# Kernel optimization log

Hardware: AMD Instinct MI355X
Metric: run time of the kernel (lower is better)

Reference implementation:

```python
import jax, jax.numpy as jnp
import numpy as np

# ---- equation / net constants (mirrors eqn_config / net_config) ----
NT = 256
DT = 0.04
N_HIST = 64
HIDDEN = 512
LAMBD = 1.0
MU1 = 0.08
MU2 = 0.02
R = 0.02
SIGMA = 0.2
BETA = 0.1
ETA = 0.5
LOGEPS = 1e-6
UTIL_PENALTY = 100.0
GEOMETRIC_SUM = (1.0 - np.exp(-LAMBD * DT * (N_HIST - 1))) / LAMBD  # discounted weight on oldest point
FINAL_DISC = float(np.exp(-BETA * NT * DT))


def setup_inputs() -> dict:
    key = jax.random.key(0)
    k = jax.random.split(key, 9)
    B = 16384
    dw_sample = jax.random.normal(k[0], (B, NT), dtype=jnp.float32) * np.sqrt(DT)
    x_init = jax.random.uniform(k[1], (B, N_HIST), dtype=jnp.float32) + 0.5  # positive initial wealth path
    # exponential kernel over the delay window (most recent point has weight ~1)
    exp_array = jnp.exp(-LAMBD * DT * jnp.arange(N_HIST - 1, 0, -1, dtype=jnp.float32))
    s1 = 1.0 / np.sqrt(N_HIST)
    s2 = 1.0 / np.sqrt(HIDDEN)
    W1 = jax.random.normal(k[2], (N_HIST, HIDDEN), dtype=jnp.float32) * s1
    b1 = jnp.zeros((HIDDEN,), dtype=jnp.float32)
    W2 = jax.random.normal(k[3], (HIDDEN, HIDDEN), dtype=jnp.float32) * s2
    b2 = jnp.zeros((HIDDEN,), dtype=jnp.float32)
    W3 = jax.random.normal(k[4], (HIDDEN, 2), dtype=jnp.float32) * s2
    b3 = jnp.zeros((2,), dtype=jnp.float32)
    return {"dw_sample": dw_sample, "x_init": x_init, "exp_array": exp_array,
            "W1": W1, "b1": b1, "W2": W2, "b2": b2, "W3": W3, "b3": b3}


def reference(dw_sample, x_init, exp_array, W1, b1, W2, b2, W3, b3):
    def util(v):  # log-utility with floor (util_tf)
        return jnp.log(jax.nn.relu(v) + LOGEPS)

    def policy(x_hist):  # feedforward policy on the history window; final_pi_tf = 2*sigmoid
        h = jax.nn.relu(x_hist @ W1 + b1)
        h = jax.nn.relu(h @ W2 + b2)
        return 2.0 * jax.nn.sigmoid(h @ W3 + b3)  # [B, 2]

    x = x_init[:, -1]                       # [B]
    x_hist0 = x_init                        # [B, N_HIST]
    y0 = jnp.sum(exp_array * x_init[:, 1:], axis=-1) * DT + GEOMETRIC_SUM * x_init[:, 0]
    reward0 = jnp.zeros_like(x)

    discounts = jnp.exp(-BETA * DT * jnp.arange(NT, dtype=jnp.float32))  # exp(-beta*t*dt)

    def step(carry, inputs):
        x, y, x_hist, reward = carry
        dw_t, disc = inputs                 # dw_t: [B], disc: scalar
        pi = policy(x_hist)                 # [B, 2]
        inst_r = util(pi[:, 0] * x) * disc - jax.nn.relu(-x) * UTIL_PENALTY
        reward = reward + inst_r * DT
        dx = ((MU1 - R) * pi[:, 1] - pi[:, 0] + R) * x + MU2 * y
        x_new = x + dx * DT + SIGMA * x * pi[:, 1] * dw_t
        y_new = y * jnp.exp(-DT * LAMBD) + x_new * DT
        x_hist_new = jnp.concatenate([x_hist[:, 1:], x_new[:, None]], axis=-1)
        return (x_new, y_new, x_hist_new, reward), None

    (x, y, _, reward), _ = jax.lax.scan(
        step, (x, y0, x_hist0, reward0), (dw_sample.T, discounts))

    # terminal step t == nt
    reward = reward + util(x + ETA * y) / BETA * FINAL_DISC
    reward = reward - jax.nn.relu(-x) * UTIL_PENALTY
    return -reward
```

## Files before the change

### kernel.cpp

```cpp
#include <hip/hip_runtime.h>
#include <stdint.h>
#include <stddef.h>

#define NTS 256

typedef short bf16x8 __attribute__((ext_vector_type(8)));
typedef short bf16x4 __attribute__((ext_vector_type(4)));
typedef float f32x4 __attribute__((ext_vector_type(4)));
typedef float f32x2 __attribute__((ext_vector_type(2)));

__device__ __forceinline__ unsigned short f2bf(float f) {
  union { float f; unsigned u; } c; c.f = f;
  unsigned u = c.u;
  u += 0x7fffu + ((u >> 16) & 1u);
  return (unsigned short)(u >> 16);
}

__global__ __launch_bounds__(256) void prep_weights(const float* __restrict__ W1,
                                                    const float* __restrict__ W2,
                                                    unsigned short* __restrict__ wp) {
  int gid = blockIdx.x * 256 + threadIdx.x;
  if (gid >= 294912) return;
  int e = gid & 7, lane = (gid >> 3) & 63, fb = (gid >> 9) & 31, pan = gid >> 14;
  int q = lane >> 4, j = lane & 15, f = fb * 16 + j;
  float v;
  if (pan < 2) v = W1[(pan * 32 + q * 8 + e) * 512 + f];
  else         v = W2[((pan - 2) * 32 + q * 8 + e) * 512 + f];
  wp[gid] = f2bf(v);
}

__device__ __forceinline__ void stage_panel(const unsigned short* __restrict__ wp,
                                            int pan, char* dst_base, int wv, int lane) {
#pragma unroll
  for (int i = 0; i < 4; ++i) {
    const unsigned short* g = wp + (size_t)pan * 16384 + (wv * 4 + i) * 512 + lane * 8;
    char* l = dst_base + wv * 4096 + i * 1024;
    __builtin_amdgcn_global_load_lds((const __attribute__((address_space(1))) void*)g,
                                     (__attribute__((address_space(3))) void*)l,
                                     16, 0, 0);
  }
}

__global__ __launch_bounds__(512, 2) void po_fused(
    const float* __restrict__ dw, const float* __restrict__ x_init,
    const float* __restrict__ exp_arr, const float* __restrict__ b1,
    const float* __restrict__ b2, const float* __restrict__ W3,
    const float* __restrict__ b3, const unsigned short* __restrict__ wp,
    float* __restrict__ out) {
  extern __shared__ char smem[];
  char* const w1L = smem;
  char* const h1C = smem + 65536;
  char* const histC = smem + 131072;
  unsigned int* const h0L = (unsigned int*)(smem + 139264);
  float* const p0L = (float*)(smem + 143360);
  float* const p1L = (float*)(smem + 145408);
  float* const dwL = (float*)(smem + 147456);
  float* const b1L = (float*)(smem + 151552);
  float* const b2L = (float*)(smem + 153600);
  float* const w3L = (float*)(smem + 155648);

  const int tid = threadIdx.x;
  const int lane = tid & 63;
  const int wv = tid >> 6;
  const int q = lane >> 4;
  const int j = lane & 15;
  const int wg = blockIdx.x;

  b1L[tid] = b1[tid];
  b2L[tid] = b2[tid];
  w3L[tid] = W3[tid];
  w3L[tid + 512] = W3[tid + 512];

  const int b_h = (wv & 3) * 16 + j;
  {
    const int k0 = (wv >> 2) * 32 + q * 8;
    const float* src = x_init + ((size_t)wg * 64 + b_h) * 64 + k0;
    bf16x8 v;
#pragma unroll
    for (int e = 0; e < 8; ++e) v[e] = (short)f2bf(src[e]);
    *(bf16x8*)(histC + tid * 16) = v;
    h0L[tid] = (unsigned int)(unsigned short)v[0];
  }

  float xreg, yreg, rreg = 0.f;
  {
    const float* row = x_init + ((size_t)wg * 64 + lane) * 64;
    float y0 = 0.f;
    for (int k = 0; k < 63; ++k) y0 += exp_arr[k] * row[1 + k];
    yreg = y0 * 0.04f + (1.f - __expf(-2.52f)) * row[0];
    xreg = row[63];
  }
  const float b30 = b3[0], b31 = b3[1];

  stage_panel(wp, 0, w1L, wv, lane);
  stage_panel(wp, 1, w1L + 32768, wv, lane);

  const unsigned short* const wpW2 = wp + 32768;
  const int wfo = wv * 2048 + lane * 8;

  bf16x8 wA[4], wB[4];
#pragma unroll
  for (int mt = 0; mt < 4; ++mt)
    wA[mt] = *(const bf16x8*)(wpW2 + wfo + mt * 512);

  __syncthreads();

  f32x4 acc[4][4];

#pragma unroll 1
  for (int t = 0; t < NTS; ++t) {
    if ((t & 15) == 0) {
      int b = tid >> 3, c = tid & 7;
      f32x2 v = *(const f32x2*)(dw + ((size_t)wg * 64 + b) * NTS + t + c * 2);
      dwL[(c * 2) * 64 + b] = v[0];
      dwL[(c * 2 + 1) * 64 + b] = v[1];
    }

#pragma unroll
    for (int mt = 0; mt < 4; ++mt)
#pragma unroll
      for (int nt = 0; nt < 4; ++nt) acc[mt][nt] = (f32x4){0.f, 0.f, 0.f, 0.f};
#pragma unroll
    for (int p = 0; p < 2; ++p) {
      const char* pb = w1L + p * 32768 + wv * 4096;
      bf16x8 bfr[4];
#pragma unroll
      for (int nt = 0; nt < 4; ++nt)
        bfr[nt] = *(const bf16x8*)(histC + ((p * 4 + nt) * 64 + lane) * 16);
#pragma unroll
      for (int mt = 0; mt < 4; ++mt) {
        bf16x8 afr = *(const bf16x8*)(pb + mt * 1024 + lane * 16);
#pragma unroll
        for (int nt = 0; nt < 4; ++nt)
          acc[mt][nt] = __builtin_amdgcn_mfma_f32_16x16x32_bf16(afr, bfr[nt],
                                                                acc[mt][nt], 0, 0, 0);
      }
    }
#pragma unroll
    for (int mt = 0; mt < 4; ++mt) {
      int f0 = wv * 64 + mt * 16 + q * 4;
      f32x4 b1v = *(const f32x4*)(b1L + f0);
      int wb = ((f0 >> 5) * 256 + ((f0 >> 3) & 3) * 16 + j) * 16 + (f0 & 7) * 2;
#pragma unroll
      for (int nt = 0; nt < 4; ++nt) {
        bf16x4 pk;
#pragma unroll
        for (int r = 0; r < 4; ++r)
          pk[r] = (short)f2bf(fmaxf(acc[mt][nt][r] + b1v[r], 0.f));
        *(bf16x4*)(h1C + wb + nt * 1024) = pk;
      }
    }
    __syncthreads();

#pragma unroll
    for (int mt = 0; mt < 4; ++mt)
#pragma unroll
      for (int nt = 0; nt < 4; ++nt) acc[mt][nt] = (f32x4){0.f, 0.f, 0.f, 0.f};
    {
      const unsigned short* pb = wpW2;
      const char* h1p = h1C;
#pragma unroll 1
      for (int kk = 0; kk < 8; ++kk) {
#pragma unroll
        for (int mt = 0; mt < 4; ++mt)
          wB[mt] = *(const bf16x8*)(pb + 16384 + wfo + mt * 512);
        __builtin_amdgcn_s_setprio(1);
#pragma unroll
        for (int nt = 0; nt < 4; ++nt) {
          bf16x8 bfr = *(const bf16x8*)(h1p + nt * 1024 + lane * 16);
#pragma unroll
          for (int mt = 0; mt < 4; ++mt)
            acc[mt][nt] = __builtin_amdgcn_mfma_f32_16x16x32_bf16(wA[mt], bfr,
                                                                  acc[mt][nt], 0, 0, 0);
        }
        __builtin_amdgcn_s_setprio(0);
        {
          const unsigned short* pn = (kk == 7) ? wpW2 : (pb + 32768);
#pragma unroll
          for (int mt = 0; mt < 4; ++mt)
            wA[mt] = *(const bf16x8*)(pn + wfo + mt * 512);
        }
        __builtin_amdgcn_s_setprio(1);
#pragma unroll
        for (int nt = 0; nt < 4; ++nt) {
          bf16x8 bfr = *(const bf16x8*)(h1p + 4096 + nt * 1024 + lane * 16);
#pragma unroll
          for (int mt = 0; mt < 4; ++mt)
            acc[mt][nt] = __builtin_amdgcn_mfma_f32_16x16x32_bf16(wB[mt], bfr,
                                                                  acc[mt][nt], 0, 0, 0);
        }
        __builtin_amdgcn_s_setprio(0);
        pb += 32768;
        h1p += 8192;
      }
    }

    {
      float p0a[4] = {0.f, 0.f, 0.f, 0.f};
      float p1a[4] = {0.f, 0.f, 0.f, 0.f};
#pragma unroll
      for (int mt = 0; mt < 4; ++mt) {
        int f0 = wv * 64 + mt * 16 + q * 4;
        f32x4 b2v = *(const f32x4*)(b2L + f0);
        f32x4 w3a = *(const f32x4*)(w3L + f0 * 2);
        f32x4 w3b = *(const f32x4*)(w3L + f0 * 2 + 4);
#pragma unroll
        for (int nt = 0; nt < 4; ++nt) {
          float v0 = fmaxf(acc[mt][nt][0] + b2v[0], 0.f);
          float v1 = fmaxf(acc[mt][nt][1] + b2v[1], 0.f);
          float v2 = fmaxf(acc[mt][nt][2] + b2v[2], 0.f);
          float v3 = fmaxf(acc[mt][nt][3] + b2v[3], 0.f);
          p0a[nt] += v0 * w3a[0] + v1 * w3a[2] + v2 * w3b[0] + v3 * w3b[2];
          p1a[nt] += v0 * w3a[1] + v1 * w3a[3] + v2 * w3b[1] + v3 * w3b[3];
        }
      }
#pragma unroll
      for (int nt = 0; nt < 4; ++nt) {
        p0a[nt] += __shfl_xor(p0a[nt], 16);
        p0a[nt] += __shfl_xor(p0a[nt], 32);
        p1a[nt] += __shfl_xor(p1a[nt], 16);
        p1a[nt] += __shfl_xor(p1a[nt], 32);
        if (q == 0) {
          int b = nt * 16 + j;
          p0L[wv * 64 + b] = p0a[nt];
          p1L[wv * 64 + b] = p1a[nt];
        }
      }
    }
    __syncthreads();

    float xn;
    {
      float z0 = b30, z1 = b31;
#pragma unroll
      for (int w = 0; w < 8; ++w) {
        z0 += p0L[w * 64 + lane];
        z1 += p1L[w * 64 + lane];
      }
      float pi0 = 2.f / (1.f + __expf(-z0));
      float pi1 = 2.f / (1.f + __expf(-z1));
      float x = xreg, y = yreg;
      float disc = __expf(-0.004f * (float)t);
      float rv = fmaxf(pi0 * x, 0.f) + 1e-6f;
      rreg += (__logf(rv) * disc - fmaxf(-x, 0.f) * 100.f) * 0.04f;
      float dwv = dwL[(t & 15) * 64 + lane];
      float dxv = (0.06f * pi1 - pi0 + 0.02f) * x + 0.02f * y;
      xn = x + dxv * 0.04f + 0.2f * x * pi1 * dwv;
      yreg = y * 0.960789439152323f + xn * 0.04f;
      xreg = xn;
    }

    {
      bf16x8 own = *(const bf16x8*)(histC + tid * 16);
      int e0 = (int)(unsigned short)own[0];
      int nbr = __shfl_down(e0, 16);
      float xb = __shfl(xn, b_h);
      unsigned short xbf = f2bf(xb);
      unsigned short last;
      if (q == 3) {
        last = (wv >= 4) ? xbf
                         : (unsigned short)h0L[(t & 1) * 512 + tid + 208];
      } else {
        last = (unsigned short)nbr;
      }
      bf16x8 nw;
#pragma unroll
      for (int e = 0; e < 7; ++e) nw[e] = own[e + 1];
      nw[7] = (short)last;
      *(bf16x8*)(histC + tid * 16) = nw;
      h0L[((t + 1) & 1) * 512 + tid] = (unsigned int)(unsigned short)nw[0];
    }
    __syncthreads();
  }

  if (tid < 64) {
    float rw = rreg + __logf(fmaxf(xreg + 0.5f * yreg, 0.f) + 1e-6f) * 10.f * __expf(-1.024f);
    rw -= fmaxf(-xreg, 0.f) * 100.f;
    out[(size_t)wg * 64 + tid] = -rw;
  }
}

extern "C" void kernel_launch(void* const* d_in, const int* in_sizes, int n_in,
                              void* d_out, int out_size, void* d_ws, size_t ws_size,
                              hipStream_t stream) {
  const float* dw      = (const float*)d_in[0];
  const float* x_init  = (const float*)d_in[1];
  const float* exp_arr = (const float*)d_in[2];
  const float* W1      = (const float*)d_in[3];
  const float* b1      = (const float*)d_in[4];
  const float* W2      = (const float*)d_in[5];
  const float* b2      = (const float*)d_in[6];
  const float* W3      = (const float*)d_in[7];
  const float* b3      = (const float*)d_in[8];
  unsigned short* wp = (unsigned short*)d_ws;
  float* out = (float*)d_out;

  (void)hipFuncSetAttribute((const void*)po_fused,
                            hipFuncAttributeMaxDynamicSharedMemorySize, 160 * 1024);

  prep_weights<<<1152, 256, 0, stream>>>(W1, W2, wp);
  po_fused<<<256, 512, 159744, stream>>>(dw, x_init, exp_arr, b1, b2, W3, b3, wp, out);
}
```

Before: 2.271 ms.

## Split W2 GEMM into two half-M passes with 4-deep weight register ring

Layer 1 is reorganized per m-tile so each tile's bias/ReLU/bf16 pack runs right after its MFMAs, and the pack uses the hardware v_cvt_pk_bf16_f32 instruction instead of software rounding. The layer-2 GEMM is split into two passes over K, each covering two of the four m-tiles, with a 4-deep ring of W2 fragments loaded from global/L2 in flight. This hides weight-load latency better. During the second pass the W3 output fold of the first half's finished accumulators is interleaved between MFMA groups, overlapping VALU work with matrix work. The cost is reading the h1 activations from LDS twice and using more registers for the deeper weight ring, which could reduce occupancy.

```diff
diff --git a/kernel.cpp b/kernel.cpp
--- a/kernel.cpp
+++ b/kernel.cpp
@@ -8,12 +8,19 @@
 typedef short bf16x4 __attribute__((ext_vector_type(4)));
 typedef float f32x4 __attribute__((ext_vector_type(4)));
 typedef float f32x2 __attribute__((ext_vector_type(2)));
+typedef unsigned int u32x2 __attribute__((ext_vector_type(2)));
 
 __device__ __forceinline__ unsigned short f2bf(float f) {
   union { float f; unsigned u; } c; c.f = f;
   unsigned u = c.u;
   u += 0x7fffu + ((u >> 16) & 1u);
   return (unsigned short)(u >> 16);
+}
+
+__device__ __forceinline__ unsigned cvt_pk_bf16(float lo, float hi) {
+  unsigned r;
+  asm("v_cvt_pk_bf16_f32 %0, %1, %2" : "=v"(r) : "v"(lo), "v"(hi));
+  return r;
 }
 
 __global__ __launch_bounds__(256) void prep_weights(const float* __restrict__ W1,
@@ -40,6 +47,19 @@
                                      16, 0, 0);
   }
 }
+
+#define FOLD_CHUNK(MT, NT) do {                                              \
+  int f0c = wv * 64 + (MT) * 16 + q * 4;                                     \
+  f32x4 b2v = *(const f32x4*)(b2L + f0c);                                    \
+  f32x4 w3a = *(const f32x4*)(w3L + f0c * 2);                                \
+  f32x4 w3b = *(const f32x4*)(w3L + f0c * 2 + 4);                            \
+  float v0 = fmaxf(acc[MT][NT][0] + b2v[0], 0.f);                            \
+  float v1 = fmaxf(acc[MT][NT][1] + b2v[1], 0.f);                            \
+  float v2 = fmaxf(acc[MT][NT][2] + b2v[2], 0.f);                            \
+  float v3 = fmaxf(acc[MT][NT][3] + b2v[3], 0.f);                            \
+  p0a[NT] += v0 * w3a[0] + v1 * w3a[2] + v2 * w3b[0] + v3 * w3b[2];          \
+  p1a[NT] += v0 * w3a[1] + v1 * w3a[3] + v2 * w3b[1] + v3 * w3b[3];          \
+} while (0)
 
 __global__ __launch_bounds__(512, 2) void po_fused(
     const float* __restrict__ dw, const float* __restrict__ x_init,
@@ -98,10 +118,12 @@
   const unsigned short* const wpW2 = wp + 32768;
   const int wfo = wv * 2048 + lane * 8;
 
-  bf16x8 wA[4], wB[4];
-#pragma unroll
-  for (int mt = 0; mt < 4; ++mt)
-    wA[mt] = *(const bf16x8*)(wpW2 + wfo + mt * 512);
+  bf16x8 wq[4][2];
+#pragma unroll
+  for (int b = 0; b < 4; ++b) {
+    wq[b][0] = *(const bf16x8*)(wpW2 + b * 16384 + wfo);
+    wq[b][1] = *(const bf16x8*)(wpW2 + b * 16384 + wfo + 512);
+  }
 
   __syncthreads();
 
@@ -116,115 +138,101 @@
       dwL[(c * 2 + 1) * 64 + b] = v[1];
     }
 
+    {
+      bf16x8 bh[8];
+#pragma unroll
+      for (int k8 = 0; k8 < 8; ++k8)
+        bh[k8] = *(const bf16x8*)(histC + (k8 * 64 + lane) * 16);
+      const char* pb0 = w1L + wv * 4096;
+#pragma unroll
+      for (int mt = 0; mt < 4; ++mt) {
+        bf16x8 af0 = *(const bf16x8*)(pb0 + mt * 1024 + lane * 16);
+        bf16x8 af1 = *(const bf16x8*)(pb0 + 32768 + mt * 1024 + lane * 16);
+        f32x4 a4[4];
+#pragma unroll
+        for (int nt = 0; nt < 4; ++nt) {
+          a4[nt] = (f32x4){0.f, 0.f, 0.f, 0.f};
+          a4[nt] = __builtin_amdgcn_mfma_f32_16x16x32_bf16(af0, bh[nt], a4[nt], 0, 0, 0);
+          a4[nt] = __builtin_amdgcn_mfma_f32_16x16x32_bf16(af1, bh[4 + nt], a4[nt], 0, 0, 0);
+        }
+        int f0 = wv * 64 + mt * 16 + q * 4;
+        f32x4 b1v = *(const f32x4*)(b1L + f0);
+        int wb = ((f0 >> 5) * 256 + ((f0 >> 3) & 3) * 16 + j) * 16 + (f0 & 7) * 2;
+#pragma unroll
+        for (int nt = 0; nt < 4; ++nt) {
+          f32x4 vv = a4[nt] + b1v;
+          u32x2 pk;
+          pk[0] = cvt_pk_bf16(fmaxf(vv[0], 0.f), fmaxf(vv[1], 0.f));
+          pk[1] = cvt_pk_bf16(fmaxf(vv[2], 0.f), fmaxf(vv[3], 0.f));
+          *(u32x2*)(h1C + wb + nt * 1024) = pk;
+        }
+      }
+    }
+    __syncthreads();
+
 #pragma unroll
     for (int mt = 0; mt < 4; ++mt)
 #pragma unroll
       for (int nt = 0; nt < 4; ++nt) acc[mt][nt] = (f32x4){0.f, 0.f, 0.f, 0.f};
-#pragma unroll
-    for (int p = 0; p < 2; ++p) {
-      const char* pb = w1L + p * 32768 + wv * 4096;
-      bf16x8 bfr[4];
-#pragma unroll
-      for (int nt = 0; nt < 4; ++nt)
-        bfr[nt] = *(const bf16x8*)(histC + ((p * 4 + nt) * 64 + lane) * 16);
-#pragma unroll
-      for (int mt = 0; mt < 4; ++mt) {
-        bf16x8 afr = *(const bf16x8*)(pb + mt * 1024 + lane * 16);
-#pragma unroll
-        for (int nt = 0; nt < 4; ++nt)
-          acc[mt][nt] = __builtin_amdgcn_mfma_f32_16x16x32_bf16(afr, bfr[nt],
-                                                                acc[mt][nt], 0, 0, 0);
-      }
-    }
-#pragma unroll
-    for (int mt = 0; mt < 4; ++mt) {
-      int f0 = wv * 64 + mt * 16 + q * 4;
-      f32x4 b1v = *(const f32x4*)(b1L + f0);
-      int wb = ((f0 >> 5) * 256 + ((f0 >> 3) & 3) * 16 + j) * 16 + (f0 & 7) * 2;
-#pragma unroll
-      for (int nt = 0; nt < 4; ++nt) {
-        bf16x4 pk;
-#pragma unroll
-        for (int r = 0; r < 4; ++r)
-          pk[r] = (short)f2bf(fmaxf(acc[mt][nt][r] + b1v[r], 0.f));
-        *(bf16x4*)(h1C + wb + nt * 1024) = pk;
-      }
-    }
-    __syncthreads();
-
-#pragma unroll
-    for (int mt = 0; mt < 4; ++mt)
-#pragma unroll
-      for (int nt = 0; nt < 4; ++nt) acc[mt][nt] = (f32x4){0.f, 0.f, 0.f, 0.f};
-    {
-      const unsigned short* pb = wpW2;
-      const char* h1p = h1C;
+    float p0a[4] = {0.f, 0.f, 0.f, 0.f};
+    float p1a[4] = {0.f, 0.f, 0.f, 0.f};
+
 #pragma unroll 1
-      for (int kk = 0; kk < 8; ++kk) {
-#pragma unroll
-        for (int mt = 0; mt < 4; ++mt)
-          wB[mt] = *(const bf16x8*)(pb + 16384 + wfo + mt * 512);
+    for (int g = 0; g < 4; ++g) {
+      const char* h1g = h1C + g * 16384;
+      const int mtsel = (g == 3) ? 1024 : 0;
+      const unsigned short* rb = wpW2 + wfo + mtsel + (((g + 1) & 3) * 4) * 16384;
+#pragma unroll
+      for (int b = 0; b < 4; ++b) {
+        const char* h1p = h1g + b * 4096;
         __builtin_amdgcn_s_setprio(1);
 #pragma unroll
         for (int nt = 0; nt < 4; ++nt) {
           bf16x8 bfr = *(const bf16x8*)(h1p + nt * 1024 + lane * 16);
-#pragma unroll
-          for (int mt = 0; mt < 4; ++mt)
-            acc[mt][nt] = __builtin_amdgcn_mfma_f32_16x16x32_bf16(wA[mt], bfr,
-                                                                  acc[mt][nt], 0, 0, 0);
+          acc[0][nt] = __builtin_amdgcn_mfma_f32_16x16x32_bf16(wq[b][0], bfr, acc[0][nt], 0, 0, 0);
+          acc[1][nt] = __builtin_amdgcn_mfma_f32_16x16x32_bf16(wq[b][1], bfr, acc[1][nt], 0, 0, 0);
         }
         __builtin_amdgcn_s_setprio(0);
-        {
-          const unsigned short* pn = (kk == 7) ? wpW2 : (pb + 32768);
-#pragma unroll
-          for (int mt = 0; mt < 4; ++mt)
-            wA[mt] = *(const bf16x8*)(pn + wfo + mt * 512);
-        }
+        wq[b][0] = *(const bf16x8*)(rb + b * 16384);
+        wq[b][1] = *(const bf16x8*)(rb + b * 16384 + 512);
+      }
+    }
+
+#pragma unroll
+    for (int g = 0; g < 4; ++g) {
+      const char* h1g = h1C + g * 16384;
+      const int mtsel = (g == 3) ? 0 : 1024;
+      const unsigned short* rb = wpW2 + wfo + mtsel + (((g + 1) & 3) * 4) * 16384;
+#pragma unroll
+      for (int b = 0; b < 4; ++b) {
+        const char* h1p = h1g + b * 4096;
         __builtin_amdgcn_s_setprio(1);
 #pragma unroll
         for (int nt = 0; nt < 4; ++nt) {
-          bf16x8 bfr = *(const bf16x8*)(h1p + 4096 + nt * 1024 + lane * 16);
-#pragma unroll
-          for (int mt = 0; mt < 4; ++mt)
-            acc[mt][nt] = __builtin_amdgcn_mfma_f32_16x16x32_bf16(wB[mt], bfr,
-                                                                  acc[mt][nt], 0, 0, 0);
+          bf16x8 bfr = *(const bf16x8*)(h1p + nt * 1024 + lane * 16);
+          acc[2][nt] = __builtin_amdgcn_mfma_f32_16x16x32_bf16(wq[b][0], bfr, acc[2][nt], 0, 0, 0);
+          acc[3][nt] = __builtin_amdgcn_mfma_f32_16x16x32_bf16(wq[b][1], bfr, acc[3][nt], 0, 0, 0);
         }
         __builtin_amdgcn_s_setprio(0);
-        pb += 32768;
-        h1p += 8192;
-      }
-    }
-
-    {
-      float p0a[4] = {0.f, 0.f, 0.f, 0.f};
-      float p1a[4] = {0.f, 0.f, 0.f, 0.f};
-#pragma unroll
-      for (int mt = 0; mt < 4; ++mt) {
-        int f0 = wv * 64 + mt * 16 + q * 4;
-        f32x4 b2v = *(const f32x4*)(b2L + f0);
-        f32x4 w3a = *(const f32x4*)(w3L + f0 * 2);
-        f32x4 w3b = *(const f32x4*)(w3L + f0 * 2 + 4);
-#pragma unroll
-        for (int nt = 0; nt < 4; ++nt) {
-          float v0 = fmaxf(acc[mt][nt][0] + b2v[0], 0.f);
-          float v1 = fmaxf(acc[mt][nt][1] + b2v[1], 0.f);
-          float v2 = fmaxf(acc[mt][nt][2] + b2v[2], 0.f);
-          float v3 = fmaxf(acc[mt][nt][3] + b2v[3], 0.f);
-          p0a[nt] += v0 * w3a[0] + v1 * w3a[2] + v2 * w3b[0] + v3 * w3b[2];
-          p1a[nt] += v0 * w3a[1] + v1 * w3a[3] + v2 * w3b[1] + v3 * w3b[3];
-        }
-      }
-#pragma unroll
-      for (int nt = 0; nt < 4; ++nt) {
-        p0a[nt] += __shfl_xor(p0a[nt], 16);
-        p0a[nt] += __shfl_xor(p0a[nt], 32);
-        p1a[nt] += __shfl_xor(p1a[nt], 16);
-        p1a[nt] += __shfl_xor(p1a[nt], 32);
-        if (q == 0) {
-          int b = nt * 16 + j;
-          p0L[wv * 64 + b] = p0a[nt];
-          p1L[wv * 64 + b] = p1a[nt];
-        }
+        wq[b][0] = *(const bf16x8*)(rb + b * 16384);
+        wq[b][1] = *(const bf16x8*)(rb + b * 16384 + 512);
+        if (b == 1) { FOLD_CHUNK((2 * g) >> 2, (2 * g) & 3); }
+        if (b == 3) { FOLD_CHUNK((2 * g + 1) >> 2, (2 * g + 1) & 3); }
+      }
+    }
+
+    FOLD_CHUNK(2, 0); FOLD_CHUNK(2, 1); FOLD_CHUNK(2, 2); FOLD_CHUNK(2, 3);
+    FOLD_CHUNK(3, 0); FOLD_CHUNK(3, 1); FOLD_CHUNK(3, 2); FOLD_CHUNK(3, 3);
+#pragma unroll
+    for (int nt = 0; nt < 4; ++nt) {
+      p0a[nt] += __shfl_xor(p0a[nt], 16);
+      p0a[nt] += __shfl_xor(p0a[nt], 32);
+      p1a[nt] += __shfl_xor(p1a[nt], 16);
+      p1a[nt] += __shfl_xor(p1a[nt], 32);
+      if (q == 0) {
+        int b = nt * 16 + j;
+        p0L[wv * 64 + b] = p0a[nt];
+        p1L[wv * 64 + b] = p1a[nt];
       }
     }
     __syncthreads();
```

Result: slower. 2.962 ms (+30.4%).

## Halve batch per block to 32, keep W1 in registers, double grid

Applied to the files above, without the earlier changes.

Each workgroup now handles 32 batch rows instead of 64, so the grid doubles to 512 blocks and the per-step work per block halves. W1 fragments move from LDS staging into registers, which cuts LDS use from about 156KB to 50KB and lets more blocks fit per CU. The ReLU-to-bf16 packing now uses the hardware v_cvt_pk_bf16_f32 instruction. The trade-off is that every block reloads all of W2 from global/L2 each step for half as many rows, which doubles total W2 traffic, and MFMA reuse per weight fragment drops.

```diff
diff --git a/kernel.cpp b/kernel.cpp
--- a/kernel.cpp
+++ b/kernel.cpp
@@ -5,15 +5,21 @@
 #define NTS 256
 
 typedef short bf16x8 __attribute__((ext_vector_type(8)));
-typedef short bf16x4 __attribute__((ext_vector_type(4)));
 typedef float f32x4 __attribute__((ext_vector_type(4)));
 typedef float f32x2 __attribute__((ext_vector_type(2)));
+typedef unsigned int u32x2 __attribute__((ext_vector_type(2)));
 
 __device__ __forceinline__ unsigned short f2bf(float f) {
   union { float f; unsigned u; } c; c.f = f;
   unsigned u = c.u;
   u += 0x7fffu + ((u >> 16) & 1u);
   return (unsigned short)(u >> 16);
+}
+
+__device__ __forceinline__ unsigned cvt_pk_bf16(float lo, float hi) {
+  unsigned r;
+  asm("v_cvt_pk_bf16_f32 %0, %1, %2" : "=v"(r) : "v"(lo), "v"(hi));
+  return r;
 }
 
 __global__ __launch_bounds__(256) void prep_weights(const float* __restrict__ W1,
@@ -29,18 +35,6 @@
   wp[gid] = f2bf(v);
 }
 
-__device__ __forceinline__ void stage_panel(const unsigned short* __restrict__ wp,
-                                            int pan, char* dst_base, int wv, int lane) {
-#pragma unroll
-  for (int i = 0; i < 4; ++i) {
-    const unsigned short* g = wp + (size_t)pan * 16384 + (wv * 4 + i) * 512 + lane * 8;
-    char* l = dst_base + wv * 4096 + i * 1024;
-    __builtin_amdgcn_global_load_lds((const __attribute__((address_space(1))) void*)g,
-                                     (__attribute__((address_space(3))) void*)l,
-                                     16, 0, 0);
-  }
-}
-
 __global__ __launch_bounds__(512, 2) void po_fused(
     const float* __restrict__ dw, const float* __restrict__ x_init,
     const float* __restrict__ exp_arr, const float* __restrict__ b1,
@@ -48,22 +42,22 @@
     const float* __restrict__ b3, const unsigned short* __restrict__ wp,
     float* __restrict__ out) {
   extern __shared__ char smem[];
-  char* const w1L = smem;
-  char* const h1C = smem + 65536;
-  char* const histC = smem + 131072;
-  unsigned int* const h0L = (unsigned int*)(smem + 139264);
-  float* const p0L = (float*)(smem + 143360);
-  float* const p1L = (float*)(smem + 145408);
-  float* const dwL = (float*)(smem + 147456);
-  float* const b1L = (float*)(smem + 151552);
-  float* const b2L = (float*)(smem + 153600);
-  float* const w3L = (float*)(smem + 155648);
+  char* const h1C = smem;
+  char* const histC = smem + 32768;
+  unsigned int* const h0L = (unsigned int*)(smem + 36864);
+  float* const p0L = (float*)(smem + 38912);
+  float* const p1L = (float*)(smem + 39936);
+  float* const dwL = (float*)(smem + 40960);
+  float* const b1L = (float*)(smem + 43008);
+  float* const b2L = (float*)(smem + 45056);
+  float* const w3L = (float*)(smem + 47104);
 
   const int tid = threadIdx.x;
   const int lane = tid & 63;
   const int wv = tid >> 6;
   const int q = lane >> 4;
   const int j = lane & 15;
+  const int rl = lane & 31;
   const int wg = blockIdx.x;
 
   b1L[tid] = b1[tid];
@@ -71,10 +65,11 @@
   w3L[tid] = W3[tid];
   w3L[tid + 512] = W3[tid + 512];
 
-  const int b_h = (wv & 3) * 16 + j;
-  {
-    const int k0 = (wv >> 2) * 32 + q * 8;
-    const float* src = x_init + ((size_t)wg * 64 + b_h) * 64 + k0;
+  const int b_colh = ((tid >> 6) & 1) * 16 + j;
+  if (tid < 256) {
+    const int p0i = (tid >> 7) & 1;
+    const int k0 = p0i * 32 + q * 8;
+    const float* src = x_init + ((size_t)wg * 32 + b_colh) * 64 + k0;
     bf16x8 v;
 #pragma unroll
     for (int e = 0; e < 8; ++e) v[e] = (short)f2bf(src[e]);
@@ -84,7 +79,7 @@
 
   float xreg, yreg, rreg = 0.f;
   {
-    const float* row = x_init + ((size_t)wg * 64 + lane) * 64;
+    const float* row = x_init + ((size_t)wg * 32 + rl) * 64;
     float y0 = 0.f;
     for (int k = 0; k < 63; ++k) y0 += exp_arr[k] * row[1 + k];
     yreg = y0 * 0.04f + (1.f - __expf(-2.52f)) * row[0];
@@ -92,8 +87,12 @@
   }
   const float b30 = b3[0], b31 = b3[1];
 
-  stage_panel(wp, 0, w1L, wv, lane);
-  stage_panel(wp, 1, w1L + 32768, wv, lane);
+  bf16x8 w1r[2][4];
+#pragma unroll
+  for (int p = 0; p < 2; ++p)
+#pragma unroll
+    for (int mt = 0; mt < 4; ++mt)
+      w1r[p][mt] = *(const bf16x8*)(wp + (((size_t)p * 32 + wv * 4 + mt) * 64 + lane) * 8);
 
   const unsigned short* const wpW2 = wp + 32768;
   const int wfo = wv * 2048 + lane * 8;
@@ -105,49 +104,46 @@
 
   __syncthreads();
 
-  f32x4 acc[4][4];
+  f32x4 acc[4][2];
 
 #pragma unroll 1
   for (int t = 0; t < NTS; ++t) {
-    if ((t & 15) == 0) {
+    if ((t & 15) == 0 && tid < 256) {
       int b = tid >> 3, c = tid & 7;
-      f32x2 v = *(const f32x2*)(dw + ((size_t)wg * 64 + b) * NTS + t + c * 2);
-      dwL[(c * 2) * 64 + b] = v[0];
-      dwL[(c * 2 + 1) * 64 + b] = v[1];
+      f32x2 v = *(const f32x2*)(dw + ((size_t)wg * 32 + b) * NTS + t + c * 2);
+      dwL[(c * 2) * 32 + b] = v[0];
+      dwL[(c * 2 + 1) * 32 + b] = v[1];
     }
 
 #pragma unroll
     for (int mt = 0; mt < 4; ++mt)
 #pragma unroll
-      for (int nt = 0; nt < 4; ++nt) acc[mt][nt] = (f32x4){0.f, 0.f, 0.f, 0.f};
+      for (int nt = 0; nt < 2; ++nt) acc[mt][nt] = (f32x4){0.f, 0.f, 0.f, 0.f};
 #pragma unroll
     for (int p = 0; p < 2; ++p) {
-      const char* pb = w1L + p * 32768 + wv * 4096;
-      bf16x8 bfr[4];
-#pragma unroll
-      for (int nt = 0; nt < 4; ++nt)
-        bfr[nt] = *(const bf16x8*)(histC + ((p * 4 + nt) * 64 + lane) * 16);
-#pragma unroll
-      for (int mt = 0; mt < 4; ++mt) {
-        bf16x8 afr = *(const bf16x8*)(pb + mt * 1024 + lane * 16);
-#pragma unroll
-        for (int nt = 0; nt < 4; ++nt)
-          acc[mt][nt] = __builtin_amdgcn_mfma_f32_16x16x32_bf16(afr, bfr[nt],
+      bf16x8 bfr[2];
+#pragma unroll
+      for (int nt = 0; nt < 2; ++nt)
+        bfr[nt] = *(const bf16x8*)(histC + ((p * 2 + nt) * 64 + lane) * 16);
+#pragma unroll
+      for (int mt = 0; mt < 4; ++mt)
+#pragma unroll
+        for (int nt = 0; nt < 2; ++nt)
+          acc[mt][nt] = __builtin_amdgcn_mfma_f32_16x16x32_bf16(w1r[p][mt], bfr[nt],
                                                                 acc[mt][nt], 0, 0, 0);
-      }
     }
 #pragma unroll
     for (int mt = 0; mt < 4; ++mt) {
       int f0 = wv * 64 + mt * 16 + q * 4;
       f32x4 b1v = *(const f32x4*)(b1L + f0);
-      int wb = ((f0 >> 5) * 256 + ((f0 >> 3) & 3) * 16 + j) * 16 + (f0 & 7) * 2;
-#pragma unroll
-      for (int nt = 0; nt < 4; ++nt) {
-        bf16x4 pk;
-#pragma unroll
-        for (int r = 0; r < 4; ++r)
-          pk[r] = (short)f2bf(fmaxf(acc[mt][nt][r] + b1v[r], 0.f));
-        *(bf16x4*)(h1C + wb + nt * 1024) = pk;
+      int wb = ((f0 >> 5) * 128 + ((f0 >> 3) & 3) * 16 + j) * 16 + (f0 & 7) * 2;
+#pragma unroll
+      for (int nt = 0; nt < 2; ++nt) {
+        f32x4 vv = acc[mt][nt] + b1v;
+        u32x2 pk;
+        pk[0] = cvt_pk_bf16(fmaxf(vv[0], 0.f), fmaxf(vv[1], 0.f));
+        pk[1] = cvt_pk_bf16(fmaxf(vv[2], 0.f), fmaxf(vv[3], 0.f));
+        *(u32x2*)(h1C + wb + nt * 1024) = pk;
       }
     }
     __syncthreads();
@@ -155,7 +151,7 @@
 #pragma unroll
     for (int mt = 0; mt < 4; ++mt)
 #pragma unroll
-      for (int nt = 0; nt < 4; ++nt) acc[mt][nt] = (f32x4){0.f, 0.f, 0.f, 0.f};
+      for (int nt = 0; nt < 2; ++nt) acc[mt][nt] = (f32x4){0.f, 0.f, 0.f, 0.f};
     {
       const unsigned short* pb = wpW2;
       const char* h1p = h1C;
@@ -166,7 +162,7 @@
           wB[mt] = *(const bf16x8*)(pb + 16384 + wfo + mt * 512);
         __builtin_amdgcn_s_setprio(1);
 #pragma unroll
-        for (int nt = 0; nt < 4; ++nt) {
+        for (int nt = 0; nt < 2; ++nt) {
           bf16x8 bfr = *(const bf16x8*)(h1p + nt * 1024 + lane * 16);
 #pragma unroll
           for (int mt = 0; mt < 4; ++mt)
@@ -182,8 +178,8 @@
         }
         __builtin_amdgcn_s_setprio(1);
 #pragma unroll
-        for (int nt = 0; nt < 4; ++nt) {
-          bf16x8 bfr = *(const bf16x8*)(h1p + 4096 + nt * 1024 + lane * 16);
+        for (int nt = 0; nt < 2; ++nt) {
+          bf16x8 bfr = *(const bf16x8*)(h1p + 2048 + nt * 1024 + lane * 16);
 #pragma unroll
           for (int mt = 0; mt < 4; ++mt)
             acc[mt][nt] = __builtin_amdgcn_mfma_f32_16x16x32_bf16(wB[mt], bfr,
@@ -191,13 +187,13 @@
         }
         __builtin_amdgcn_s_setprio(0);
         pb += 32768;
-        h1p += 8192;
+        h1p += 4096;
       }
     }
 
     {
-      float p0a[4] = {0.f, 0.f, 0.f, 0.f};
-      float p1a[4] = {0.f, 0.f, 0.f, 0.f};
+      float p0a[2] = {0.f, 0.f};
+      float p1a[2] = {0.f, 0.f};
 #pragma unroll
       for (int mt = 0; mt < 4; ++mt) {
         int f0 = wv * 64 + mt * 16 + q * 4;
@@ -205,7 +201,7 @@
         f32x4 w3a = *(const f32x4*)(w3L + f0 * 2);
         f32x4 w3b = *(const f32x4*)(w3L + f0 * 2 + 4);
 #pragma unroll
-        for (int nt = 0; nt < 4; ++nt) {
+        for (int nt = 0; nt < 2; ++nt) {
           float v0 = fmaxf(acc[mt][nt][0] + b2v[0], 0.f);
           float v1 = fmaxf(acc[mt][nt][1] + b2v[1], 0.f);
           float v2 = fmaxf(acc[mt][nt][2] + b2v[2], 0.f);
@@ -215,15 +211,15 @@
         }
       }
 #pragma unroll
-      for (int nt = 0; nt < 4; ++nt) {
+      for (int nt = 0; nt < 2; ++nt) {
         p0a[nt] += __shfl_xor(p0a[nt], 16);
         p0a[nt] += __shfl_xor(p0a[nt], 32);
         p1a[nt] += __shfl_xor(p1a[nt], 16);
         p1a[nt] += __shfl_xor(p1a[nt], 32);
         if (q == 0) {
           int b = nt * 16 + j;
-          p0L[wv * 64 + b] = p0a[nt];
-          p1L[wv * 64 + b] = p1a[nt];
+          p0L[wv * 32 + b] = p0a[nt];
+          p1L[wv * 32 + b] = p1a[nt];
         }
       }
     }
@@ -234,8 +230,8 @@
       float z0 = b30, z1 = b31;
 #pragma unroll
       for (int w = 0; w < 8; ++w) {
-        z0 += p0L[w * 64 + lane];
-        z1 += p1L[w * 64 + lane];
+        z0 += p0L[w * 32 + rl];
+        z1 += p1L[w * 32 + rl];
       }
       float pi0 = 2.f / (1.f + __expf(-z0));
       float pi1 = 2.f / (1.f + __expf(-z1));
@@ -243,23 +239,24 @@
       float disc = __expf(-0.004f * (float)t);
       float rv = fmaxf(pi0 * x, 0.f) + 1e-6f;
       rreg += (__logf(rv) * disc - fmaxf(-x, 0.f) * 100.f) * 0.04f;
-      float dwv = dwL[(t & 15) * 64 + lane];
+      float dwv = dwL[(t & 15) * 32 + rl];
       float dxv = (0.06f * pi1 - pi0 + 0.02f) * x + 0.02f * y;
       xn = x + dxv * 0.04f + 0.2f * x * pi1 * dwv;
       yreg = y * 0.960789439152323f + xn * 0.04f;
       xreg = xn;
     }
 
-    {
+    if (tid < 256) {
       bf16x8 own = *(const bf16x8*)(histC + tid * 16);
       int e0 = (int)(unsigned short)own[0];
       int nbr = __shfl_down(e0, 16);
-      float xb = __shfl(xn, b_h);
+      float xb = __shfl(xn, b_colh);
       unsigned short xbf = f2bf(xb);
+      const int pIdx = (tid >> 7) & 1;
       unsigned short last;
       if (q == 3) {
-        last = (wv >= 4) ? xbf
-                         : (unsigned short)h0L[(t & 1) * 512 + tid + 208];
+        last = (pIdx == 1) ? xbf
+                           : (unsigned short)h0L[(t & 1) * 256 + tid + 80];
       } else {
         last = (unsigned short)nbr;
       }
@@ -268,15 +265,15 @@
       for (int e = 0; e < 7; ++e) nw[e] = own[e + 1];
       nw[7] = (short)last;
       *(bf16x8*)(histC + tid * 16) = nw;
-      h0L[((t + 1) & 1) * 512 + tid] = (unsigned int)(unsigned short)nw[0];
+      h0L[((t + 1) & 1) * 256 + tid] = (unsigned int)(unsigned short)nw[0];
     }
     __syncthreads();
   }
 
-  if (tid < 64) {
+  if (tid < 32) {
     float rw = rreg + __logf(fmaxf(xreg + 0.5f * yreg, 0.f) + 1e-6f) * 10.f * __expf(-1.024f);
     rw -= fmaxf(-xreg, 0.f) * 100.f;
-    out[(size_t)wg * 64 + tid] = -rw;
+    out[(size_t)wg * 32 + tid] = -rw;
   }
 }
 
@@ -299,5 +296,5 @@
                             hipFuncAttributeMaxDynamicSharedMemorySize, 160 * 1024);
 
   prep_weights<<<1152, 256, 0, stream>>>(W1, W2, wp);
-  po_fused<<<256, 512, 159744, stream>>>(dw, x_init, exp_arr, b1, b2, W3, b3, wp, out);
-}
+  po_fused<<<512, 512, 51200, stream>>>(dw, x_init, exp_arr, b1, b2, W3, b3, wp, out);
+}
```

After: 2.900 ms. +27.7%, slower.
